# Kernel optimization log

Hardware: AMD Instinct MI355X
Metric: run time of the kernel (lower is better)

Reference implementation:

```python
import jax, jax.numpy as jnp
import numpy as np

B, L, D, DK, T = 8192, 64, 512, 64, 128
WIDE_IN = 2 * T + T * T  # 16640


def setup_inputs() -> dict:
    key = jax.random.key(0)
    ks = jax.random.split(key, 24)
    s = 0.02
    inp = {
        "mashup_tags": jax.random.uniform(ks[0], (B, T), jnp.float32),
        "target_api_tags": jax.random.uniform(ks[1], (B, T), jnp.float32),
        "cross_product_tag": jax.random.uniform(ks[2], (B, T * T), jnp.float32),
        "encoded_api_context": jax.random.normal(ks[3], (B, L, D), jnp.float32),
        "candidate_api_description_feature": jax.random.normal(ks[4], (B, D), jnp.float32),
        "mashup_description_feature": jax.random.normal(ks[5], (B, D), jnp.float32),
        "context_len": jax.random.randint(ks[6], (B,), 0, L + 1, jnp.int64 if jax.config.jax_enable_x64 else jnp.int32),
        # attention projections (torch Linear weight layout: [out, in], no bias)
        "W_K": s * jax.random.normal(ks[7], (DK, D), jnp.float32),
        "W_Q": s * jax.random.normal(ks[8], (DK, D), jnp.float32),
        # wide head
        "wide_w": s * jax.random.normal(ks[9], (1, WIDE_IN), jnp.float32),
        "wide_b": jnp.zeros((1,), jnp.float32),
        # deep MLP 1536->512->256->128->1
        "d1_w": s * jax.random.normal(ks[10], (512, 3 * D), jnp.float32),
        "d1_b": jnp.zeros((512,), jnp.float32),
        "d2_w": s * jax.random.normal(ks[11], (256, 512), jnp.float32),
        "d2_b": jnp.zeros((256,), jnp.float32),
        "d3_w": s * jax.random.normal(ks[12], (128, 256), jnp.float32),
        "d3_b": jnp.zeros((128,), jnp.float32),
        "d4_w": s * jax.random.normal(ks[13], (1, 128), jnp.float32),
        "d4_b": jnp.zeros((1,), jnp.float32),
        "wide_weight": jnp.ones((1,), jnp.float32),
        "deep_weight": jnp.ones((1,), jnp.float32),
        "bias": jnp.zeros((1,), jnp.float32),
    }
    return inp


def reference(mashup_tags, target_api_tags, cross_product_tag,
              encoded_api_context, candidate_api_description_feature,
              mashup_description_feature, context_len,
              W_K, W_Q, wide_w, wide_b,
              d1_w, d1_b, d2_w, d2_b, d3_w, d3_b, d4_w, d4_b,
              wide_weight, deep_weight, bias):
    # ---- wide branch ----
    wide_in = jnp.concatenate([mashup_tags, target_api_tags, cross_product_tag], axis=1)
    wide_out = jax.nn.sigmoid(wide_in @ wide_w.T + wide_b)  # (B,1)

    # ---- ragged attention (vectorized masked softmax replaces the Python batch loop) ----
    K = jnp.einsum("bld,kd->blk", encoded_api_context, W_K)          # (B,L,dk)
    Q = candidate_api_description_feature @ W_Q.T                     # (B,dk)
    scores = jnp.einsum("blk,bk->bl", K, Q)                           # (B,L)
    mask = jnp.arange(scores.shape[1])[None, :] < context_len[:, None]
    m = jnp.max(jnp.where(mask, scores, -1e30), axis=-1, keepdims=True)
    e = jnp.where(mask, jnp.exp(scores - m), 0.0)
    denom = jnp.sum(e, axis=-1, keepdims=True)
    probs = e / jnp.maximum(denom, 1e-30)  # rows with length==0 -> all zeros (matches torch zeros fallback)
    api_context = jnp.einsum("bl,bld->bd", probs, encoded_api_context)  # (B,512)

    # ---- deep branch ----
    deep_in = jnp.concatenate([mashup_description_feature, api_context,
                               candidate_api_description_feature], axis=1)  # (B,1536)
    h = jax.nn.relu(deep_in @ d1_w.T + d1_b)
    h = jax.nn.relu(h @ d2_w.T + d2_b)
    h = jax.nn.relu(h @ d3_w.T + d3_b)
    deep_out = h @ d4_w.T + d4_b  # (B,1)

    out = wide_weight * wide_out + deep_weight * deep_out + bias
    return jax.nn.sigmoid(out)
```

## Files before the change

### kernel.cpp

```cpp
#include <hip/hip_runtime.h>

#define Bsz 8192
#define Lctx 64
#define Ddim 512
#define DK 64
#define Ttag 128
#define RQT 2

using f32x4 = __attribute__((ext_vector_type(4))) float;
using bf16x8 = __attribute__((ext_vector_type(8))) short;

__device__ __forceinline__ float wave_sum(float v) {
#pragma unroll
    for (int m = 32; m > 0; m >>= 1) v += __shfl_xor(v, m, 64);
    return v;
}

__device__ __forceinline__ float dot4(float4 a, float4 b) {
    return a.x * b.x + a.y * b.y + a.z * b.z + a.w * b.w;
}

__device__ __forceinline__ unsigned f2bf(float f) {
    unsigned int u = __float_as_uint(f);
    u = u + 0x7fffu + ((u >> 16) & 1u);
    return u >> 16;
}
__device__ __forceinline__ unsigned pack2(float a, float b) {
    return f2bf(a) | (f2bf(b) << 16);
}
__device__ __forceinline__ float bflo(unsigned int v) { return __uint_as_float(v << 16); }
__device__ __forceinline__ float bfhi(unsigned int v) { return __uint_as_float(v & 0xffff0000u); }
__device__ __forceinline__ float bf2f(unsigned short u) { return __uint_as_float((unsigned)u << 16); }

__global__ __launch_bounds__(256) void k_f2bf3(
    const float* __restrict__ s1, unsigned short* __restrict__ d1,
    const float* __restrict__ s2, unsigned short* __restrict__ d2,
    const float* __restrict__ s3, unsigned short* __restrict__ d3)
{
    int i = blockIdx.x * 256 + threadIdx.x;
    const float* s;
    unsigned short* d;
    if (i < 196608)      { s = s1; d = d1; }
    else if (i < 229376) { i -= 196608; s = s2; d = d2; }
    else if (i < 237568) { i -= 229376; s = s3; d = d3; }
    else return;
    const float4 v = ((const float4*)s)[i];
    uint2 w;
    w.x = pack2(v.x, v.y);
    w.y = pack2(v.z, v.w);
    *(uint2*)&d[(size_t)i * 4] = w;
}

__global__ __launch_bounds__(256) void k_qtilde(
    const float* __restrict__ C, const float* __restrict__ WQ,
    const float* __restrict__ WK, float* __restrict__ qt)
{
    const int lane = threadIdx.x & 63;
    const int gw = blockIdx.x * 4 + (threadIdx.x >> 6);
    const int b0 = gw * RQT;

    float4 c0[RQT], c1[RQT];
#pragma unroll
    for (int r = 0; r < RQT; ++r) {
        const float4* row = (const float4*)(C + (size_t)(b0 + r) * Ddim);
        c0[r] = row[lane];
        c1[r] = row[64 + lane];
    }
    float tv[RQT];
#pragma unroll
    for (int r = 0; r < RQT; ++r) tv[r] = 0.f;
    for (int k = 0; k < DK; ++k) {
        const float4* wrow = (const float4*)(WQ + (size_t)k * Ddim);
        const float4 w0 = wrow[lane];
        const float4 w1 = wrow[64 + lane];
#pragma unroll
        for (int r = 0; r < RQT; ++r) {
            float p = dot4(c0[r], w0) + dot4(c1[r], w1);
            p = wave_sum(p);
            if (lane == k) tv[r] = p;
        }
    }
    float4 a0[RQT], a1[RQT];
#pragma unroll
    for (int r = 0; r < RQT; ++r) {
        a0[r] = make_float4(0.f, 0.f, 0.f, 0.f);
        a1[r] = make_float4(0.f, 0.f, 0.f, 0.f);
    }
    for (int k = 0; k < DK; ++k) {
        const float4* wrow = (const float4*)(WK + (size_t)k * Ddim);
        const float4 w0 = wrow[lane];
        const float4 w1 = wrow[64 + lane];
#pragma unroll
        for (int r = 0; r < RQT; ++r) {
            const float tk = __shfl(tv[r], k, 64);
            a0[r].x += tk * w0.x; a0[r].y += tk * w0.y;
            a0[r].z += tk * w0.z; a0[r].w += tk * w0.w;
            a1[r].x += tk * w1.x; a1[r].y += tk * w1.y;
            a1[r].z += tk * w1.z; a1[r].w += tk * w1.w;
        }
    }
#pragma unroll
    for (int r = 0; r < RQT; ++r) {
        float4* orow = (float4*)(qt + (size_t)(b0 + r) * Ddim);
        orow[lane] = a0[r];
        orow[64 + lane] = a1[r];
    }
}

__global__ __launch_bounds__(512, 2) void k_attn_wide(
    const float* __restrict__ X, const float* __restrict__ qt,
    const int* __restrict__ clen, const float* __restrict__ mdesc,
    const float* __restrict__ cand,
    const float* __restrict__ mt, const float* __restrict__ tt,
    const float* __restrict__ cp, const float* __restrict__ ww,
    const float* __restrict__ wb,
    unsigned short* __restrict__ din, float* __restrict__ wl)
{
    __shared__ float sl[Lctx];
    __shared__ float pl[Lctx];
    __shared__ float part[8][Ddim];
    __shared__ float red[8];

    const int b = blockIdx.x;
    const int tid = threadIdx.x;
    const int wave = tid >> 6, lane = tid & 63;
    const int len = clen[b];
    const int nrows = min(8, max(0, len - wave * 8));

    const float4* qrow = (const float4*)(qt + (size_t)b * Ddim);
    const float4 q0 = qrow[lane];
    const float4 q1 = qrow[64 + lane];
    const float4* xb = (const float4*)(X + (size_t)b * Lctx * Ddim);

    uint2 pk[8][2];
    float sc[8];

    if (nrows > 0) {
        float4 t0[8], t1[8];
#pragma unroll
        for (int r = 0; r < 8; ++r) {
            const int l = wave * 8 + min(r, nrows - 1);
            t0[r] = xb[l * 128 + lane];
            t1[r] = xb[l * 128 + 64 + lane];
        }
#pragma unroll
        for (int r = 0; r < 8; ++r) {
            if (r < nrows) {
                sc[r] = dot4(t0[r], q0) + dot4(t1[r], q1);
                pk[r][0].x = pack2(t0[r].x, t0[r].y);
                pk[r][0].y = pack2(t0[r].z, t0[r].w);
                pk[r][1].x = pack2(t1[r].x, t1[r].y);
                pk[r][1].y = pack2(t1[r].z, t1[r].w);
            }
        }
#pragma unroll
        for (int r = 0; r < 8; ++r)
            if (r < nrows) sc[r] = wave_sum(sc[r]);
        if (lane == 0) {
#pragma unroll
            for (int r = 0; r < 8; ++r)
                if (r < nrows) sl[wave * 8 + r] = sc[r];
        }
    }

    float wacc = 0.f;
    if (tid < 64) {
        float4 v;
        if (tid < 32) v = ((const float4*)(mt + (size_t)b * Ttag))[tid];
        else          v = ((const float4*)(tt + (size_t)b * Ttag))[tid - 32];
        wacc += dot4(v, ((const float4*)ww)[tid]);
    }
    {
        const float4* cp4 = (const float4*)(cp + (size_t)b * (Ttag * Ttag));
        const float4* ww4 = (const float4*)(ww + 2 * Ttag);
#pragma unroll 4
        for (int i = tid; i < (Ttag * Ttag) / 4; i += 512)
            wacc += dot4(cp4[i], ww4[i]);
    }
    wacc = wave_sum(wacc);
    if (lane == 0) red[wave] = wacc;

    __syncthreads();

    if (wave == 0) {
        const float s = (lane < len) ? sl[lane] : -1e30f;
        float m = s;
#pragma unroll
        for (int msk = 32; msk > 0; msk >>= 1)
            m = fmaxf(m, __shfl_xor(m, msk, 64));
        const float e = (lane < len) ? __expf(s - m) : 0.f;
        const float d = wave_sum(e);
        pl[lane] = e * (1.f / fmaxf(d, 1e-30f));
    }
    __syncthreads();

    float4 a0 = make_float4(0.f, 0.f, 0.f, 0.f);
    float4 a1 = make_float4(0.f, 0.f, 0.f, 0.f);
#pragma unroll
    for (int r = 0; r < 8; ++r) {
        if (r < nrows) {
            const float p = pl[wave * 8 + r];
            a0.x += p * bflo(pk[r][0].x); a0.y += p * bfhi(pk[r][0].x);
            a0.z += p * bflo(pk[r][0].y); a0.w += p * bfhi(pk[r][0].y);
            a1.x += p * bflo(pk[r][1].x); a1.y += p * bfhi(pk[r][1].x);
            a1.z += p * bflo(pk[r][1].y); a1.w += p * bfhi(pk[r][1].y);
        }
    }
    *(float4*)&part[wave][lane * 4] = a0;
    *(float4*)&part[wave][256 + lane * 4] = a1;
    __syncthreads();

    unsigned short* dr = din + (size_t)b * 1536;
    {
        float v = 0.f;
#pragma unroll
        for (int w8 = 0; w8 < 8; ++w8) v += part[w8][tid];
        dr[512 + tid] = (unsigned short)f2bf(v);
    }
    if (tid < 256) {
        const float4 v = (tid < 128)
            ? ((const float4*)(mdesc + (size_t)b * Ddim))[tid]
            : ((const float4*)(cand + (size_t)b * Ddim))[tid - 128];
        uint2 w;
        w.x = pack2(v.x, v.y);
        w.y = pack2(v.z, v.w);
        const int off = (tid < 128) ? tid * 4 : 1024 + (tid - 128) * 4;
        *(uint2*)&dr[off] = w;
    }
    if (tid == 0)
        wl[b] = red[0] + red[1] + red[2] + red[3] +
                red[4] + red[5] + red[6] + red[7] + wb[0];
}

__global__ __launch_bounds__(256) void k_gemm_bf16(
    const unsigned short* __restrict__ A, const unsigned short* __restrict__ W,
    const float* __restrict__ bias, unsigned short* __restrict__ C,
    const int K, const int N, const int relu)
{
    __shared__ unsigned short As[128][72];
    __shared__ unsigned short Bs[128][72];
    const int tid = threadIdx.x;
    const int wave = tid >> 6, lane = tid & 63;
    const int wm = wave >> 1, wn = wave & 1;
    const size_t m0 = (size_t)blockIdx.x * 128;
    const size_t n0 = (size_t)blockIdx.y * 128;

    f32x4 acc[4][4];
#pragma unroll
    for (int i = 0; i < 4; ++i)
#pragma unroll
        for (int j = 0; j < 4; ++j) acc[i][j] = (f32x4){0.f, 0.f, 0.f, 0.f};

    uint4 pa[4], pb[4];
    auto loadA = [&](int k0) {
#pragma unroll
        for (int j = 0; j < 4; ++j) {
            const int i = tid + j * 256;
            const int row = i >> 3, c8 = (i & 7) * 8;
            pa[j] = *(const uint4*)(A + (m0 + row) * (size_t)K + k0 + c8);
        }
    };
    auto loadB = [&](int k0) {
#pragma unroll
        for (int j = 0; j < 4; ++j) {
            const int i = tid + j * 256;
            const int row = i >> 3, c8 = (i & 7) * 8;
            pb[j] = *(const uint4*)(W + (n0 + row) * (size_t)K + k0 + c8);
        }
    };

    loadA(0);
    loadB(0);
    for (int k0 = 0; k0 < K; k0 += 64) {
        __syncthreads();
#pragma unroll
        for (int j = 0; j < 4; ++j) {
            const int i = tid + j * 256;
            const int row = i >> 3, c8 = (i & 7) * 8;
            *(uint4*)&As[row][c8] = pa[j];
            *(uint4*)&Bs[row][c8] = pb[j];
        }
        __syncthreads();
        if (k0 + 64 < K) { loadA(k0 + 64); loadB(k0 + 64); }
#pragma unroll
        for (int kk = 0; kk < 2; ++kk) {
            const int krow = kk * 32 + (lane >> 4) * 8;
            bf16x8 af[4], bfr[4];
#pragma unroll
            for (int mm = 0; mm < 4; ++mm)
                af[mm] = *(const bf16x8*)&As[wm * 64 + mm * 16 + (lane & 15)][krow];
#pragma unroll
            for (int nn = 0; nn < 4; ++nn)
                bfr[nn] = *(const bf16x8*)&Bs[wn * 64 + nn * 16 + (lane & 15)][krow];
#pragma unroll
            for (int mm = 0; mm < 4; ++mm)
#pragma unroll
                for (int nn = 0; nn < 4; ++nn)
                    acc[mm][nn] = __builtin_amdgcn_mfma_f32_16x16x32_bf16(
                        af[mm], bfr[nn], acc[mm][nn], 0, 0, 0);
        }
    }

#pragma unroll
    for (int nn = 0; nn < 4; ++nn) {
        const int col = (int)n0 + wn * 64 + nn * 16 + (lane & 15);
        const float bv = bias[col];
#pragma unroll
        for (int mm = 0; mm < 4; ++mm) {
#pragma unroll
            for (int r = 0; r < 4; ++r) {
                const size_t row = m0 + wm * 64 + mm * 16 + (lane >> 4) * 4 + r;
                float v = acc[mm][nn][r] + bv;
                if (relu) v = fmaxf(v, 0.f);
                C[row * N + col] = (unsigned short)f2bf(v);
            }
        }
    }
}

__global__ __launch_bounds__(256) void k_final(
    const unsigned short* __restrict__ h3, const float* __restrict__ d4w,
    const float* __restrict__ d4b, const float* __restrict__ wl,
    const float* __restrict__ wwt, const float* __restrict__ dwt,
    const float* __restrict__ bs, float* __restrict__ out)
{
    const int lane = threadIdx.x & 63;
    const int b = blockIdx.x * 4 + (threadIdx.x >> 6);
    const unsigned short* hr = h3 + (size_t)b * 128;
    float v = bf2f(hr[lane]) * d4w[lane] + bf2f(hr[64 + lane]) * d4w[64 + lane];
    v = wave_sum(v);
    if (lane == 0) {
        const float deep = v + d4b[0];
        const float wo = 1.f / (1.f + __expf(-wl[b]));
        const float z = wwt[0] * wo + dwt[0] * deep + bs[0];
        out[b] = 1.f / (1.f + __expf(-z));
    }
}

extern "C" void kernel_launch(void* const* d_in, const int* in_sizes, int n_in,
                              void* d_out, int out_size, void* d_ws, size_t ws_size,
                              hipStream_t stream)
{
    const float* mt    = (const float*)d_in[0];
    const float* tt    = (const float*)d_in[1];
    const float* cp    = (const float*)d_in[2];
    const float* X     = (const float*)d_in[3];
    const float* cand  = (const float*)d_in[4];
    const float* mdesc = (const float*)d_in[5];
    const int*   clen  = (const int*)d_in[6];
    const float* WK    = (const float*)d_in[7];
    const float* WQ    = (const float*)d_in[8];
    const float* ww    = (const float*)d_in[9];
    const float* wb    = (const float*)d_in[10];
    const float* d1w   = (const float*)d_in[11];
    const float* d1b   = (const float*)d_in[12];
    const float* d2w   = (const float*)d_in[13];
    const float* d2b   = (const float*)d_in[14];
    const float* d3w   = (const float*)d_in[15];
    const float* d3b   = (const float*)d_in[16];
    const float* d4w   = (const float*)d_in[17];
    const float* d4b   = (const float*)d_in[18];
    const float* wwt   = (const float*)d_in[19];
    const float* dwt   = (const float*)d_in[20];
    const float* bs    = (const float*)d_in[21];
    float* out = (float*)d_out;

    char* w = (char*)d_ws;
    unsigned short* din = (unsigned short*)w;            w += (size_t)Bsz * 1536 * 2;
    float* qt           = (float*)w;                     w += (size_t)Bsz * 512 * 4;
    unsigned short* h1  = (unsigned short*)w;            w += (size_t)Bsz * 512 * 2;
    unsigned short* h2  = (unsigned short*)w;            w += (size_t)Bsz * 256 * 2;
    unsigned short* h3  = (unsigned short*)w;            w += (size_t)Bsz * 128 * 2;
    float* wl           = (float*)w;                     w += (size_t)Bsz * 4;
    unsigned short* w1b = (unsigned short*)w;            w += (size_t)512 * 1536 * 2;
    unsigned short* w2b = (unsigned short*)w;            w += (size_t)256 * 512 * 2;
    unsigned short* w3b = (unsigned short*)w;            w += (size_t)128 * 256 * 2;

    hipLaunchKernelGGL(k_f2bf3, dim3(928), dim3(256), 0, stream,
                       d1w, w1b, d2w, w2b, d3w, w3b);
    hipLaunchKernelGGL(k_qtilde, dim3(Bsz / (RQT * 4)), dim3(256), 0, stream,
                       cand, WQ, WK, qt);
    hipLaunchKernelGGL(k_attn_wide, dim3(Bsz), dim3(512), 0, stream,
                       X, qt, clen, mdesc, cand, mt, tt, cp, ww, wb, din, wl);
    hipLaunchKernelGGL(k_gemm_bf16, dim3(64, 4), dim3(256), 0, stream,
                       din, w1b, d1b, h1, 1536, 512, 1);
    hipLaunchKernelGGL(k_gemm_bf16, dim3(64, 2), dim3(256), 0, stream,
                       h1, w2b, d2b, h2, 512, 256, 1);
    hipLaunchKernelGGL(k_gemm_bf16, dim3(64, 1), dim3(256), 0, stream,
                       h2, w3b, d3b, h3, 256, 128, 1);
    hipLaunchKernelGGL(k_final, dim3(Bsz / 4), dim3(256), 0, stream,
                       h3, d4w, d4b, wl, wwt, dwt, bs, out);
}
```

Before: 407.1 us.

## Map one wave per batch row with online softmax in attention-wide kernel

```diff
diff --git a/kernel.cpp b/kernel.cpp
--- a/kernel.cpp
+++ b/kernel.cpp
@@ -5,7 +5,7 @@
 #define Ddim 512
 #define DK 64
 #define Ttag 128
-#define RQT 2
+#define RQT 4
 
 using f32x4 = __attribute__((ext_vector_type(4))) float;
 using bf16x8 = __attribute__((ext_vector_type(8))) short;
@@ -28,8 +28,6 @@
 __device__ __forceinline__ unsigned pack2(float a, float b) {
     return f2bf(a) | (f2bf(b) << 16);
 }
-__device__ __forceinline__ float bflo(unsigned int v) { return __uint_as_float(v << 16); }
-__device__ __forceinline__ float bfhi(unsigned int v) { return __uint_as_float(v & 0xffff0000u); }
 __device__ __forceinline__ float bf2f(unsigned short u) { return __uint_as_float((unsigned)u << 16); }
 
 __global__ __launch_bounds__(256) void k_f2bf3(
@@ -107,7 +105,7 @@
     }
 }
 
-__global__ __launch_bounds__(512, 2) void k_attn_wide(
+__global__ __launch_bounds__(256, 4) void k_attn_wide(
     const float* __restrict__ X, const float* __restrict__ qt,
     const int* __restrict__ clen, const float* __restrict__ mdesc,
     const float* __restrict__ cand,
@@ -116,120 +114,112 @@
     const float* __restrict__ wb,
     unsigned short* __restrict__ din, float* __restrict__ wl)
 {
-    __shared__ float sl[Lctx];
-    __shared__ float pl[Lctx];
-    __shared__ float part[8][Ddim];
-    __shared__ float red[8];
-
-    const int b = blockIdx.x;
     const int tid = threadIdx.x;
     const int wave = tid >> 6, lane = tid & 63;
+    const int b = blockIdx.x * 4 + wave;
     const int len = clen[b];
-    const int nrows = min(8, max(0, len - wave * 8));
 
     const float4* qrow = (const float4*)(qt + (size_t)b * Ddim);
     const float4 q0 = qrow[lane];
     const float4 q1 = qrow[64 + lane];
     const float4* xb = (const float4*)(X + (size_t)b * Lctx * Ddim);
 
-    uint2 pk[8][2];
-    float sc[8];
-
-    if (nrows > 0) {
+    float4 y0 = make_float4(0.f, 0.f, 0.f, 0.f);
+    float4 y1 = make_float4(0.f, 0.f, 0.f, 0.f);
+    float M = -1e30f, D = 0.f;
+
+    const int nch = (len + 7) >> 3;
+    for (int c = 0; c < nch; ++c) {
+        const int base = c * 8;
+        const int nr = min(8, len - base);
         float4 t0[8], t1[8];
 #pragma unroll
         for (int r = 0; r < 8; ++r) {
-            const int l = wave * 8 + min(r, nrows - 1);
+            const int l = base + min(r, nr - 1);
             t0[r] = xb[l * 128 + lane];
             t1[r] = xb[l * 128 + 64 + lane];
         }
+        float sc[8];
+#pragma unroll
+        for (int r = 0; r < 8; ++r)
+            sc[r] = dot4(t0[r], q0) + dot4(t1[r], q1);
+#pragma unroll
+        for (int r = 0; r < 8; ++r) sc[r] = wave_sum(sc[r]);
+
+        float pmax = -1e30f;
+#pragma unroll
+        for (int r = 0; r < 8; ++r)
+            if (r < nr) pmax = fmaxf(pmax, sc[r]);
+        const float Mn = fmaxf(M, pmax);
+        const float scale = __expf(M - Mn);
+        D *= scale;
+        y0.x *= scale; y0.y *= scale; y0.z *= scale; y0.w *= scale;
+        y1.x *= scale; y1.y *= scale; y1.z *= scale; y1.w *= scale;
 #pragma unroll
         for (int r = 0; r < 8; ++r) {
-            if (r < nrows) {
-                sc[r] = dot4(t0[r], q0) + dot4(t1[r], q1);
-                pk[r][0].x = pack2(t0[r].x, t0[r].y);
-                pk[r][0].y = pack2(t0[r].z, t0[r].w);
-                pk[r][1].x = pack2(t1[r].x, t1[r].y);
-                pk[r][1].y = pack2(t1[r].z, t1[r].w);
+            if (r < nr) {
+                const float e = __expf(sc[r] - Mn);
+                D += e;
+                y0.x += e * t0[r].x; y0.y += e * t0[r].y;
+                y0.z += e * t0[r].z; y0.w += e * t0[r].w;
+                y1.x += e * t1[r].x; y1.y += e * t1[r].y;
+                y1.z += e * t1[r].z; y1.w += e * t1[r].w;
             }
         }
-#pragma unroll
-        for (int r = 0; r < 8; ++r)
-            if (r < nrows) sc[r] = wave_sum(sc[r]);
-        if (lane == 0) {
-#pragma unroll
-            for (int r = 0; r < 8; ++r)
-                if (r < nrows) sl[wave * 8 + r] = sc[r];
-        }
-    }
-
-    float wacc = 0.f;
-    if (tid < 64) {
-        float4 v;
-        if (tid < 32) v = ((const float4*)(mt + (size_t)b * Ttag))[tid];
-        else          v = ((const float4*)(tt + (size_t)b * Ttag))[tid - 32];
-        wacc += dot4(v, ((const float4*)ww)[tid]);
+        M = Mn;
+    }
+
+    float wacc;
+    {
+        const float2 a  = ((const float2*)(mt + (size_t)b * Ttag))[lane];
+        const float2 wA = ((const float2*)ww)[lane];
+        const float2 t  = ((const float2*)(tt + (size_t)b * Ttag))[lane];
+        const float2 wB = ((const float2*)(ww + Ttag))[lane];
+        wacc = a.x * wA.x + a.y * wA.y + t.x * wB.x + t.y * wB.y;
     }
     {
         const float4* cp4 = (const float4*)(cp + (size_t)b * (Ttag * Ttag));
         const float4* ww4 = (const float4*)(ww + 2 * Ttag);
-#pragma unroll 4
-        for (int i = tid; i < (Ttag * Ttag) / 4; i += 512)
-            wacc += dot4(cp4[i], ww4[i]);
+        float wa = 0.f, wbk = 0.f;
+#pragma unroll 8
+        for (int i = 0; i < 64; i += 2) {
+            wa  += dot4(cp4[i * 64 + lane],       ww4[i * 64 + lane]);
+            wbk += dot4(cp4[(i + 1) * 64 + lane], ww4[(i + 1) * 64 + lane]);
+        }
+        wacc += wa + wbk;
     }
     wacc = wave_sum(wacc);
-    if (lane == 0) red[wave] = wacc;
-
-    __syncthreads();
-
-    if (wave == 0) {
-        const float s = (lane < len) ? sl[lane] : -1e30f;
-        float m = s;
-#pragma unroll
-        for (int msk = 32; msk > 0; msk >>= 1)
-            m = fmaxf(m, __shfl_xor(m, msk, 64));
-        const float e = (lane < len) ? __expf(s - m) : 0.f;
-        const float d = wave_sum(e);
-        pl[lane] = e * (1.f / fmaxf(d, 1e-30f));
-    }
-    __syncthreads();
-
-    float4 a0 = make_float4(0.f, 0.f, 0.f, 0.f);
-    float4 a1 = make_float4(0.f, 0.f, 0.f, 0.f);
-#pragma unroll
-    for (int r = 0; r < 8; ++r) {
-        if (r < nrows) {
-            const float p = pl[wave * 8 + r];
-            a0.x += p * bflo(pk[r][0].x); a0.y += p * bfhi(pk[r][0].x);
-            a0.z += p * bflo(pk[r][0].y); a0.w += p * bfhi(pk[r][0].y);
-            a1.x += p * bflo(pk[r][1].x); a1.y += p * bfhi(pk[r][1].x);
-            a1.z += p * bflo(pk[r][1].y); a1.w += p * bfhi(pk[r][1].y);
-        }
-    }
-    *(float4*)&part[wave][lane * 4] = a0;
-    *(float4*)&part[wave][256 + lane * 4] = a1;
-    __syncthreads();
+    if (lane == 0) wl[b] = wacc + wb[0];
 
     unsigned short* dr = din + (size_t)b * 1536;
-    {
-        float v = 0.f;
-#pragma unroll
-        for (int w8 = 0; w8 < 8; ++w8) v += part[w8][tid];
-        dr[512 + tid] = (unsigned short)f2bf(v);
-    }
-    if (tid < 256) {
-        const float4 v = (tid < 128)
-            ? ((const float4*)(mdesc + (size_t)b * Ddim))[tid]
-            : ((const float4*)(cand + (size_t)b * Ddim))[tid - 128];
+    const float rden = 1.f / fmaxf(D, 1e-30f);
+    {
         uint2 w;
-        w.x = pack2(v.x, v.y);
-        w.y = pack2(v.z, v.w);
-        const int off = (tid < 128) ? tid * 4 : 1024 + (tid - 128) * 4;
-        *(uint2*)&dr[off] = w;
-    }
-    if (tid == 0)
-        wl[b] = red[0] + red[1] + red[2] + red[3] +
-                red[4] + red[5] + red[6] + red[7] + wb[0];
+        w.x = pack2(y0.x * rden, y0.y * rden);
+        w.y = pack2(y0.z * rden, y0.w * rden);
+        *(uint2*)&dr[512 + 4 * lane] = w;
+        w.x = pack2(y1.x * rden, y1.y * rden);
+        w.y = pack2(y1.z * rden, y1.w * rden);
+        *(uint2*)&dr[512 + 256 + 4 * lane] = w;
+    }
+    {
+        const float4* md = (const float4*)(mdesc + (size_t)b * Ddim);
+        const float4 m0 = md[lane], m1 = md[64 + lane];
+        uint2 w;
+        w.x = pack2(m0.x, m0.y); w.y = pack2(m0.z, m0.w);
+        *(uint2*)&dr[4 * lane] = w;
+        w.x = pack2(m1.x, m1.y); w.y = pack2(m1.z, m1.w);
+        *(uint2*)&dr[256 + 4 * lane] = w;
+    }
+    {
+        const float4* cd = (const float4*)(cand + (size_t)b * Ddim);
+        const float4 c0 = cd[lane], c1 = cd[64 + lane];
+        uint2 w;
+        w.x = pack2(c0.x, c0.y); w.y = pack2(c0.z, c0.w);
+        *(uint2*)&dr[1024 + 4 * lane] = w;
+        w.x = pack2(c1.x, c1.y); w.y = pack2(c1.z, c1.w);
+        *(uint2*)&dr[1024 + 256 + 4 * lane] = w;
+    }
 }
 
 __global__ __launch_bounds__(256) void k_gemm_bf16(
@@ -380,7 +370,7 @@
                        d1w, w1b, d2w, w2b, d3w, w3b);
     hipLaunchKernelGGL(k_qtilde, dim3(Bsz / (RQT * 4)), dim3(256), 0, stream,
                        cand, WQ, WK, qt);
-    hipLaunchKernelGGL(k_attn_wide, dim3(Bsz), dim3(512), 0, stream,
+    hipLaunchKernelGGL(k_attn_wide, dim3(Bsz / 4), dim3(256), 0, stream,
                        X, qt, clen, mdesc, cand, mt, tt, cp, ww, wb, din, wl);
     hipLaunchKernelGGL(k_gemm_bf16, dim3(64, 4), dim3(256), 0, stream,
                        din, w1b, d1b, h1, 1536, 512, 1);
```

After: 438.5 us. 7.7% more time.
